# Kernel tuning notes

Hardware: AMD Instinct MI355X
Metric: run time of the kernel (lower is better)

The kernel has to match this reference:

```python
import jax, jax.numpy as jnp
import numpy as np

N = 50000      # nodes
E = 800000     # edges
D = 128        # in = out features (required by Euler residual update)
GRID_SIZE = 5
K = 3          # spline order
GRID_LO, GRID_HI = -1.0, 1.0
EPSILON = 0.001
NUM_BASES = GRID_SIZE + K  # 8


def make_grid(in_features):
    # extended uniform grid: [in, grid_size + 2k + 1]
    h = (GRID_HI - GRID_LO) / GRID_SIZE
    g = jnp.arange(-K, GRID_SIZE + K + 1, dtype=jnp.float32) * h + GRID_LO
    return jnp.broadcast_to(g, (in_features, g.shape[0]))


def b_splines(x, grid):
    # x: [N, in]; grid: [in, g+2k+1] -> bases: [N, in, g+k] (Cox-de Boor)
    xe = x[..., None]
    bases = ((xe >= grid[:, :-1]) & (xe < grid[:, 1:])).astype(x.dtype)
    for j in range(1, K + 1):
        left = (xe - grid[:, : -(j + 1)]) / (grid[:, j:-1] - grid[:, : -(j + 1)])
        right = (grid[:, j + 1:] - xe) / (grid[:, j + 1:] - grid[:, 1:-j])
        bases = left * bases[..., :-1] + right * bases[..., 1:]
    return bases


def kan_transform(x, base_w, spline_w, grid):
    # efficient-KAN layer (scale_and_bias=False): silu base branch + spline branch
    base = jax.nn.silu(x) @ base_w.T                    # [N, out]
    sb = b_splines(x, grid)                             # [N, in, g+k]
    spl = jnp.einsum('nib,oib->no', sb, spline_w)       # [N, out]
    return base + spl


def gcn_norm_coeffs(edge_index, n):
    # A_hat symmetric normalization: deg includes self-loop (+1)
    src, dst = edge_index[0], edge_index[1]
    deg = jnp.zeros((n,), jnp.float32).at[dst].add(1.0) + 1.0
    dis = jax.lax.rsqrt(deg)
    return dis[src] * dis[dst]


def setup_inputs() -> dict:
    key = jax.random.key(0)
    ks = jax.random.split(key, 6)
    x = jax.random.uniform(ks[0], (N, D), jnp.float32) * 2.0 - 1.0  # in grid_range
    edge_index = jax.random.randint(ks[1], (2, E), 0, N, dtype=jnp.int64)
    base_w_l = jax.random.normal(ks[2], (D, D), jnp.float32) * (1.0 / np.sqrt(D))
    spline_w_l = jax.random.normal(ks[3], (D, D, NUM_BASES), jnp.float32) * 0.1
    base_w_c = jax.random.normal(ks[4], (D, D), jnp.float32) * (1.0 / np.sqrt(D))
    spline_w_c = jax.random.normal(ks[5], (D, D, NUM_BASES), jnp.float32) * 0.1
    return {"x": x, "edge_index": edge_index, "base_w_l": base_w_l,
            "spline_w_l": spline_w_l, "base_w_c": base_w_c,
            "spline_w_c": spline_w_c, "delta_t": 2}


def reference(x, edge_index, base_w_l, spline_w_l, base_w_c, spline_w_c, delta_t):
    grid = make_grid(D)
    src, dst = edge_index[0], edge_index[1]
    norm = gcn_norm_coeffs(edge_index, N)  # [E]

    def layer(h):
        # KANLayer branch on node features
        h_l = kan_transform(h, base_w_l, spline_w_l, grid)
        # KANConv branch: aggregate_first -> normalized scatter-add, then KAN
        msgs = norm[:, None] * h[src]                              # [E, D]
        agg = jax.ops.segment_sum(msgs, dst, num_segments=N)       # [N, D]
        h_c = kan_transform(agg, base_w_c, spline_w_c, grid)
        return h_l + h_c

    for _ in range(int(delta_t)):   # explicit Euler ODE steps
        x = x + EPSILON * layer(x)
    return x
```

## Files before the change

kernel.cpp:

```cpp
#include <hip/hip_runtime.h>
#include <hip/hip_bf16.h>

#define NNODES 50000
#define NEDGES 800000
#define DF 128
#define KW 1152
#define EPS 0.001f
#define NB 196

typedef __bf16 bf16x8 __attribute__((ext_vector_type(8)));
typedef __bf16 bf16x4 __attribute__((ext_vector_type(4)));
typedef float  f32x4  __attribute__((ext_vector_type(4)));
typedef unsigned long ulongx2 __attribute__((ext_vector_type(2)));

#define GLOAD16(g, l) __builtin_amdgcn_global_load_lds( \
    (const __attribute__((address_space(1))) unsigned int*)(g), \
    (__attribute__((address_space(3))) unsigned int*)(l), 16, 0, 0)

__global__ void prep_fused(const float* __restrict__ x, const int* __restrict__ ei,
                           const float* __restrict__ bwl, const float* __restrict__ swl,
                           const float* __restrict__ bwc, const float* __restrict__ swc,
                           __bf16* __restrict__ xb, int* __restrict__ deg,
                           __bf16* __restrict__ wtl, __bf16* __restrict__ wtc) {
    const int bid = blockIdx.x;
    if (bid < 3125) {
        int i = bid * 256 + threadIdx.x;
        f32x4 a = ((const f32x4*)x)[2 * i];
        f32x4 b = ((const f32x4*)x)[2 * i + 1];
        bf16x8 o;
        o[0] = (__bf16)a[0]; o[1] = (__bf16)a[1]; o[2] = (__bf16)a[2]; o[3] = (__bf16)a[3];
        o[4] = (__bf16)b[0]; o[5] = (__bf16)b[1]; o[6] = (__bf16)b[2]; o[7] = (__bf16)b[3];
        ((bf16x8*)xb)[i] = o;
        atomicAdd(&deg[ei[NEDGES + i]], 1);
    } else {
        int idx = (bid - 3125) * 256 + threadIdx.x;
        int half = idx / (DF * KW);
        int gid  = idx - half * (DF * KW);
        const float* bw = half ? bwc : bwl;
        const float* sw = half ? swc : swl;
        __bf16*      wt = half ? wtc : wtl;
        int o = gid / KW;
        int k = gid - o * KW;
        float v = (k < 128) ? bw[o * DF + k] : sw[o * 1024 + (k - 128)];
        wt[gid] = (__bf16)v;
    }
}

__global__ void scan_part(const int* __restrict__ deg, int* __restrict__ bsum) {
    __shared__ int red[256];
    int t = threadIdx.x;
    int i = blockIdx.x * 256 + t;
    red[t] = (i < NNODES) ? deg[i] : 0;
    __syncthreads();
    for (int off = 128; off > 0; off >>= 1) {
        if (t < off) red[t] += red[t + off];
        __syncthreads();
    }
    if (t == 0) bsum[blockIdx.x] = red[0];
}

__global__ void scan_bsum(const int* __restrict__ bsum, int* __restrict__ boff) {
    __shared__ int buf[256];
    int t = threadIdx.x;
    int v = (t < NB) ? bsum[t] : 0;
    buf[t] = v;
    __syncthreads();
    for (int off = 1; off < 256; off <<= 1) {
        int x = (t >= off) ? buf[t - off] : 0;
        __syncthreads();
        buf[t] += x;
        __syncthreads();
    }
    if (t <= NB) boff[t] = buf[t] - ((t < NB) ? bsum[t] : 0);
}

__global__ void scan_final(const int* __restrict__ deg, const int* __restrict__ boff,
                           int* __restrict__ rowptr) {
    __shared__ int buf[256];
    int t = threadIdx.x;
    int i = blockIdx.x * 256 + t;
    int v = (i < NNODES) ? deg[i] : 0;
    buf[t] = v;
    __syncthreads();
    for (int off = 1; off < 256; off <<= 1) {
        int x = (t >= off) ? buf[t - off] : 0;
        __syncthreads();
        buf[t] += x;
        __syncthreads();
    }
    if (i < NNODES) rowptr[i] = buf[t] - v + boff[blockIdx.x];
    if (blockIdx.x == 0 && t == 0) rowptr[NNODES] = boff[NB];
}

__global__ void fill_csr(const int* __restrict__ ei, const int* __restrict__ deg,
                         const int* __restrict__ rowptr, int* __restrict__ cnt,
                         int* __restrict__ esrc, float* __restrict__ ew) {
    int e = blockIdx.x * 256 + threadIdx.x;
    if (e >= NEDGES) return;
    int s = ei[e];
    int d = ei[NEDGES + e];
    float w = rsqrtf((float)(deg[s] + 1)) * rsqrtf((float)(deg[d] + 1));
    int p = rowptr[d] + atomicAdd(&cnt[d], 1);
    esrc[p] = s;
    ew[p] = w;
}

__global__ __launch_bounds__(256) void agg_gather(
        const int* __restrict__ rowptr, const int* __restrict__ esrc,
        const float* __restrict__ ew, const __bf16* __restrict__ hb,
        __bf16* __restrict__ aggb) {
    const int tid = blockIdx.x * 256 + threadIdx.x;
    const int n = tid >> 4;
    const int l = tid & 15;
    if (n >= NNODES) return;
    int p  = rowptr[n];
    const int pe = rowptr[n + 1];
    float acc[8] = {};
    int   cs0, cs1, cs2, cs3;
    float cw0, cw1, cw2, cw3;
    bool have = (p + 3 < pe);
    if (have) {
        cs0 = esrc[p]; cs1 = esrc[p + 1]; cs2 = esrc[p + 2]; cs3 = esrc[p + 3];
        cw0 = ew[p];   cw1 = ew[p + 1];   cw2 = ew[p + 2];   cw3 = ew[p + 3];
    }
    while (have) {
        int np = p + 4;
        bool nh = (np + 3 < pe);
        int   ns0 = 0, ns1 = 0, ns2 = 0, ns3 = 0;
        float nw0 = 0, nw1 = 0, nw2 = 0, nw3 = 0;
        if (nh) {
            ns0 = esrc[np]; ns1 = esrc[np + 1]; ns2 = esrc[np + 2]; ns3 = esrc[np + 3];
            nw0 = ew[np];   nw1 = ew[np + 1];   nw2 = ew[np + 2];   nw3 = ew[np + 3];
        }
        bf16x8 v0 = *(const bf16x8*)(hb + (size_t)cs0 * DF + l * 8);
        bf16x8 v1 = *(const bf16x8*)(hb + (size_t)cs1 * DF + l * 8);
        bf16x8 v2 = *(const bf16x8*)(hb + (size_t)cs2 * DF + l * 8);
        bf16x8 v3 = *(const bf16x8*)(hb + (size_t)cs3 * DF + l * 8);
#pragma unroll
        for (int j = 0; j < 8; ++j)
            acc[j] += cw0 * (float)v0[j] + cw1 * (float)v1[j]
                    + cw2 * (float)v2[j] + cw3 * (float)v3[j];
        p = np;
        cs0 = ns0; cs1 = ns1; cs2 = ns2; cs3 = ns3;
        cw0 = nw0; cw1 = nw1; cw2 = nw2; cw3 = nw3;
        have = nh;
    }
    for (; p < pe; ++p) {
        int   s0 = esrc[p];
        float w0 = ew[p];
        bf16x8 v0 = *(const bf16x8*)(hb + (size_t)s0 * DF + l * 8);
#pragma unroll
        for (int j = 0; j < 8; ++j) acc[j] += w0 * (float)v0[j];
    }
    bf16x8 o;
#pragma unroll
    for (int j = 0; j < 8; ++j) o[j] = (__bf16)acc[j];
    *(bf16x8*)(aggb + (size_t)n * DF + l * 8) = o;
}

__global__ __launch_bounds__(256, 4) void kan_step(
        const float* __restrict__ h,
        const __bf16* __restrict__ xb,
        const __bf16* __restrict__ aggb,
        const __bf16* __restrict__ wtl, const __bf16* __restrict__ wtc,
        float* __restrict__ out, __bf16* __restrict__ outb) {
    __shared__ __bf16 Bs[3][128 * 32];
    __shared__ __bf16 Xs[64 * 128];

    const int tid  = threadIdx.x;
    const int lane = tid & 63;
    const int w    = tid >> 6;
    const int q    = lane >> 4, l15 = lane & 15;
    const int n0   = blockIdx.x * 64;
    const int myrow = w * 16 + l15;
    const int msw   = myrow & 7;

    const int relrow = lane >> 2;
    const int slotx  = (lane & 3) ^ ((relrow >> 1) & 3);
    const int r0 = w * 16 + relrow;
    const size_t gb0 = (size_t)r0 * KW + (size_t)slotx * 8;
    const size_t gb1 = gb0 + (size_t)64 * KW;

    const int bslot = (q ^ ((l15 >> 1) & 3)) * 8;

    const int xrow = tid >> 2, xseg = tid & 3;
    const bool xok = (n0 + xrow) < NNODES;
    const size_t xgoff = (size_t)(n0 + xrow) * DF + xseg * 32;

    f32x4 acc[8] = {};

    auto xs_write = [&](uint4 v0, uint4 v1, uint4 v2, uint4 v3) {
        const int gl = xrow * 16 + xseg * 4;
        const int sw = xrow & 7;
        *(uint4*)&Xs[(size_t)((gl + 0) ^ sw) * 8] = v0;
        *(uint4*)&Xs[(size_t)((gl + 1) ^ sw) * 8] = v1;
        *(uint4*)&Xs[(size_t)((gl + 2) ^ sw) * 8] = v2;
        *(uint4*)&Xs[(size_t)((gl + 3) ^ sw) * 8] = v3;
    };

    auto stageB = [&](int t2, int sb) {
        const __bf16* wtp = (t2 >= 36) ? wtc : wtl;
        const int k0 = ((t2 >= 36) ? t2 - 36 : t2) * 32;
        GLOAD16(wtp + gb0 + k0, &Bs[sb][(w * 16) * 32]);
        GLOAD16(wtp + gb1 + k0, &Bs[sb][(64 + w * 16) * 32]);
    };

    auto spline_pack = [&](float x) -> bf16x8 {
        float f  = __builtin_fmaf(x, 2.5f, 5.5f);
        float fi = floorf(f);
        int  idx = (int)fi;
        float u  = f - fi;
        float u2 = u * u, u3 = u2 * u;
        float om = 1.0f - u;
        float Wa = u3 * (1.0f / 6.0f);
        float Wb = (((-3.0f * u + 3.0f) * u + 3.0f) * u + 1.0f) * (1.0f / 6.0f);
        float Wc = ((3.0f * u - 6.0f) * u2 + 4.0f) * (1.0f / 6.0f);
        float Wd = om * om * om * (1.0f / 6.0f);
        unsigned long p =
              (unsigned long)__builtin_bit_cast(unsigned short, (__bf16)Wd)
            | ((unsigned long)__builtin_bit_cast(unsigned short, (__bf16)Wc) << 16)
            | ((unsigned long)__builtin_bit_cast(unsigned short, (__bf16)Wb) << 32)
            | ((unsigned long)__builtin_bit_cast(unsigned short, (__bf16)Wa) << 48);
        int tt = idx - 3;
        unsigned long lo, hi;
        if (tt >= 0) {
            int s = (tt & 3) * 16;
            unsigned long sv = p << s;
            unsigned long cr = (p >> (63 - s)) >> 1;
            bool hh = tt >= 4;
            lo = hh ? 0ul : sv;
            hi = hh ? sv : cr;
            if (tt >= 8) { lo = 0; hi = 0; }
        } else {
            int s = (-tt) * 16;
            lo = (tt >= -3) ? (p >> (s & 63)) : 0ul;
            hi = 0;
        }
        ulongx2 r; r[0] = lo; r[1] = hi;
        return __builtin_bit_cast(bf16x8, r);
    };

    auto silu8 = [&](const __bf16* xs) -> bf16x8 {
        bf16x8 v = *(const bf16x8*)xs;
        bf16x8 o;
#pragma unroll
        for (int j = 0; j < 8; ++j) {
            float x = (float)v[j];
            o[j] = (__bf16)(x / (1.0f + __expf(-x)));
        }
        return o;
    };

    uint4 a0 = {}, a1 = {}, a2 = {}, a3 = {};
    uint4 c0 = {}, c1 = {}, c2 = {}, c3 = {};
    if (xok) {
        const uint4* ga = (const uint4*)(xb + xgoff);
        a0 = ga[0]; a1 = ga[1]; a2 = ga[2]; a3 = ga[3];
        const uint4* gc = (const uint4*)(aggb + xgoff);
        c0 = gc[0]; c1 = gc[1]; c2 = gc[2]; c3 = gc[3];
    }
    xs_write(a0, a1, a2, a3);
    stageB(0, 0);
    stageB(1, 1);
    asm volatile("s_waitcnt lgkmcnt(0)" ::: "memory");

    auto body = [&](int t, int cb, int sb, bool doStage, bool last) {
        if (last) asm volatile("s_waitcnt vmcnt(0)" ::: "memory");
        else      asm volatile("s_waitcnt vmcnt(2)" ::: "memory");
        __builtin_amdgcn_s_barrier();
        __builtin_amdgcn_sched_barrier(0);

        if (t == 36) {
            xs_write(c0, c1, c2, c3);
            asm volatile("s_waitcnt lgkmcnt(0)" ::: "memory");
            __builtin_amdgcn_s_barrier();
            __builtin_amdgcn_sched_barrier(0);
        }

        if (doStage) stageB(t + 2, sb);

        const int ck = (t >= 36) ? t - 36 : t;
        bf16x8 a;
        if (ck < 4) {
            const int g = (myrow * 16 + ck * 4 + q) ^ msw;
            a = silu8(&Xs[(size_t)g * 8]);
        } else {
            const int f = (ck - 4) * 4 + q;
            const int g = (myrow * 16 + (f >> 3)) ^ msw;
            unsigned short u0 =
                *(const unsigned short*)&Xs[(size_t)g * 8 + (f & 7)];
            a = spline_pack(__builtin_bit_cast(float, (unsigned)u0 << 16));
        }

        bf16x8 bF[8];
#pragma unroll
        for (int nj = 0; nj < 8; ++nj)
            bF[nj] = *(const bf16x8*)&Bs[cb][(nj * 16 + l15) * 32 + bslot];
#pragma unroll
        for (int nj = 0; nj < 8; ++nj)
            acc[nj] = __builtin_amdgcn_mfma_f32_16x16x32_bf16(a, bF[nj], acc[nj], 0, 0, 0);
    };

    int cb = 0, sb = 2;
#pragma unroll 3
    for (int t = 0; t < 69; ++t) {
        body(t, cb, sb, true, false);
        cb = (cb == 2) ? 0 : cb + 1;
        sb = (sb == 2) ? 0 : sb + 1;
    }
    body(69, 0, 2, true,  false);
    body(70, 1, 0, false, false);
    body(71, 2, 0, false, true);

    const bool wxb = (outb != nullptr);
#pragma unroll
    for (int nj = 0; nj < 8; ++nj) {
#pragma unroll
        for (int r = 0; r < 4; ++r) {
            int row = n0 + w * 16 + q * 4 + r;
            int col = nj * 16 + l15;
            if (row < NNODES) {
                size_t idx = (size_t)row * DF + col;
                float v = h[idx] + EPS * acc[nj][r];
                out[idx] = v;
                if (wxb) outb[idx] = (__bf16)v;
            }
        }
    }
}

extern "C" void kernel_launch(void* const* d_in, const int* in_sizes, int n_in,
                              void* d_out, int out_size, void* d_ws, size_t ws_size,
                              hipStream_t stream) {
    const float* x   = (const float*)d_in[0];
    const int*   ei  = (const int*)d_in[1];
    const float* bwl = (const float*)d_in[2];
    const float* swl = (const float*)d_in[3];
    const float* bwc = (const float*)d_in[4];
    const float* swc = (const float*)d_in[5];
    float* out = (float*)d_out;

    char* ws = (char*)d_ws;
    int*    deg    = (int*)  (ws + 0);
    int*    cnt    = (int*)  (ws + 200000);
    int*    rowptr = (int*)  (ws + 400000);
    int*    bsum   = (int*)  (ws + 600064);
    int*    boff   = (int*)  (ws + 600896);
    int*    esrc   = (int*)  (ws + 601728);
    float*  ew     = (float*)(ws + 3801728);
    __bf16* xb     = (__bf16*)(ws + 7001728);
    __bf16* aggb   = (__bf16*)(ws + 19801728);
    __bf16* wtl    = (__bf16*)(ws + 32601728);
    __bf16* wtc    = (__bf16*)(ws + 32896640);

    (void)hipMemsetAsync(deg, 0, 400000, stream);
    prep_fused<<<4277, 256, 0, stream>>>(x, ei, bwl, swl, bwc, swc, xb, deg, wtl, wtc);
    scan_part<<<NB, 256, 0, stream>>>(deg, bsum);
    scan_bsum<<<1, 256, 0, stream>>>(bsum, boff);
    scan_final<<<NB, 256, 0, stream>>>(deg, boff, rowptr);
    fill_csr<<<3125, 256, 0, stream>>>(ei, deg, rowptr, cnt, esrc, ew);

    const int gemm_grid = (NNODES + 63) / 64;
    agg_gather<<<3125, 256, 0, stream>>>(rowptr, esrc, ew, xb, aggb);
    kan_step<<<gemm_grid, 256, 0, stream>>>(x, xb, aggb, wtl, wtc, out, xb);
    agg_gather<<<3125, 256, 0, stream>>>(rowptr, esrc, ew, xb, aggb);
    kan_step<<<gemm_grid, 256, 0, stream>>>(out, xb, aggb, wtl, wtc, out, (__bf16*)nullptr);
}
```

Baseline: 370.3 us.

## Co-schedule KAN-layer GEMM with edge aggregation in one interleaved kernel

Splits the combined KAN step into two parts. The node-feature KAN-layer GEMM, which needs no aggregation, now runs inside the gather kernel: one block in five does GEMM tiles while the others aggregate, so compute-bound and memory-bound work share the GPU. The result is stored as a bf16 partial sum. The second kernel then runs only the conv-branch GEMM and adds that partial at writeback. The cost is an extra bf16 round trip through global memory, rounding of the partial to bf16, and LDS allocated even for aggregation blocks, which may limit their occupancy.

```diff
diff --git a/kernel.cpp b/kernel.cpp
--- a/kernel.cpp
+++ b/kernel.cpp
@@ -9,7 +9,6 @@
 #define NB 196
 
 typedef __bf16 bf16x8 __attribute__((ext_vector_type(8)));
-typedef __bf16 bf16x4 __attribute__((ext_vector_type(4)));
 typedef float  f32x4  __attribute__((ext_vector_type(4)));
 typedef unsigned long ulongx2 __attribute__((ext_vector_type(2)));
 
@@ -105,64 +104,214 @@
     ew[p] = w;
 }
 
-__global__ __launch_bounds__(256) void agg_gather(
+__device__ __forceinline__ bf16x8 spline_pack(float x) {
+    float f  = __builtin_fmaf(x, 2.5f, 5.5f);
+    float fi = floorf(f);
+    int  idx = (int)fi;
+    float u  = f - fi;
+    float u2 = u * u, u3 = u2 * u;
+    float om = 1.0f - u;
+    float Wa = u3 * (1.0f / 6.0f);
+    float Wb = (((-3.0f * u + 3.0f) * u + 3.0f) * u + 1.0f) * (1.0f / 6.0f);
+    float Wc = ((3.0f * u - 6.0f) * u2 + 4.0f) * (1.0f / 6.0f);
+    float Wd = om * om * om * (1.0f / 6.0f);
+    unsigned long p =
+          (unsigned long)__builtin_bit_cast(unsigned short, (__bf16)Wd)
+        | ((unsigned long)__builtin_bit_cast(unsigned short, (__bf16)Wc) << 16)
+        | ((unsigned long)__builtin_bit_cast(unsigned short, (__bf16)Wb) << 32)
+        | ((unsigned long)__builtin_bit_cast(unsigned short, (__bf16)Wa) << 48);
+    int tt = idx - 3;
+    unsigned long lo, hi;
+    if (tt >= 0) {
+        int s = (tt & 3) * 16;
+        unsigned long sv = p << s;
+        unsigned long cr = (p >> (63 - s)) >> 1;
+        bool hh = tt >= 4;
+        lo = hh ? 0ul : sv;
+        hi = hh ? sv : cr;
+        if (tt >= 8) { lo = 0; hi = 0; }
+    } else {
+        int s = (-tt) * 16;
+        lo = (tt >= -3) ? (p >> (s & 63)) : 0ul;
+        hi = 0;
+    }
+    ulongx2 r; r[0] = lo; r[1] = hi;
+    return __builtin_bit_cast(bf16x8, r);
+}
+
+__device__ __forceinline__ bf16x8 silu8p(const __bf16* xs) {
+    bf16x8 v = *(const bf16x8*)xs;
+    bf16x8 o;
+#pragma unroll
+    for (int j = 0; j < 8; ++j) {
+        float x = (float)v[j];
+        o[j] = (__bf16)(x / (1.0f + __expf(-x)));
+    }
+    return o;
+}
+
+__global__ __launch_bounds__(256, 4) void agg_kanl(
         const int* __restrict__ rowptr, const int* __restrict__ esrc,
-        const float* __restrict__ ew, const __bf16* __restrict__ hb,
-        __bf16* __restrict__ aggb) {
-    const int tid = blockIdx.x * 256 + threadIdx.x;
-    const int n = tid >> 4;
-    const int l = tid & 15;
-    if (n >= NNODES) return;
-    int p  = rowptr[n];
-    const int pe = rowptr[n + 1];
-    float acc[8] = {};
-    int   cs0, cs1, cs2, cs3;
-    float cw0, cw1, cw2, cw3;
-    bool have = (p + 3 < pe);
-    if (have) {
-        cs0 = esrc[p]; cs1 = esrc[p + 1]; cs2 = esrc[p + 2]; cs3 = esrc[p + 3];
-        cw0 = ew[p];   cw1 = ew[p + 1];   cw2 = ew[p + 2];   cw3 = ew[p + 3];
-    }
-    while (have) {
-        int np = p + 4;
-        bool nh = (np + 3 < pe);
-        int   ns0 = 0, ns1 = 0, ns2 = 0, ns3 = 0;
-        float nw0 = 0, nw1 = 0, nw2 = 0, nw3 = 0;
-        if (nh) {
-            ns0 = esrc[np]; ns1 = esrc[np + 1]; ns2 = esrc[np + 2]; ns3 = esrc[np + 3];
-            nw0 = ew[np];   nw1 = ew[np + 1];   nw2 = ew[np + 2];   nw3 = ew[np + 3];
-        }
-        bf16x8 v0 = *(const bf16x8*)(hb + (size_t)cs0 * DF + l * 8);
-        bf16x8 v1 = *(const bf16x8*)(hb + (size_t)cs1 * DF + l * 8);
-        bf16x8 v2 = *(const bf16x8*)(hb + (size_t)cs2 * DF + l * 8);
-        bf16x8 v3 = *(const bf16x8*)(hb + (size_t)cs3 * DF + l * 8);
-#pragma unroll
-        for (int j = 0; j < 8; ++j)
-            acc[j] += cw0 * (float)v0[j] + cw1 * (float)v1[j]
-                    + cw2 * (float)v2[j] + cw3 * (float)v3[j];
-        p = np;
-        cs0 = ns0; cs1 = ns1; cs2 = ns2; cs3 = ns3;
-        cw0 = nw0; cw1 = nw1; cw2 = nw2; cw3 = nw3;
-        have = nh;
-    }
-    for (; p < pe; ++p) {
-        int   s0 = esrc[p];
-        float w0 = ew[p];
-        bf16x8 v0 = *(const bf16x8*)(hb + (size_t)s0 * DF + l * 8);
-#pragma unroll
-        for (int j = 0; j < 8; ++j) acc[j] += w0 * (float)v0[j];
-    }
-    bf16x8 o;
-#pragma unroll
-    for (int j = 0; j < 8; ++j) o[j] = (__bf16)acc[j];
-    *(bf16x8*)(aggb + (size_t)n * DF + l * 8) = o;
-}
-
-__global__ __launch_bounds__(256, 4) void kan_step(
+        const float* __restrict__ ew, const __bf16* __restrict__ xb,
+        __bf16* __restrict__ aggb, const __bf16* __restrict__ wtl,
+        __bf16* __restrict__ accb) {
+    __shared__ __bf16 Bs[3][128 * 32];
+    __shared__ __bf16 Xs[64 * 128];
+
+    const int bid = blockIdx.x;
+    const int k5 = bid / 5, r5 = bid - k5 * 5;
+    const bool isKanl = (r5 == 4) || (bid == 3906);
+
+    if (!isKanl) {
+        const int ablk = k5 * 4 + r5;
+        const int vtid = ablk * 256 + threadIdx.x;
+        const int n = vtid >> 4;
+        const int l = vtid & 15;
+        if (n >= NNODES) return;
+        int p  = rowptr[n];
+        const int pe = rowptr[n + 1];
+        float acc[8] = {};
+        int   cs0, cs1, cs2, cs3;
+        float cw0, cw1, cw2, cw3;
+        bool have = (p + 3 < pe);
+        if (have) {
+            cs0 = esrc[p]; cs1 = esrc[p + 1]; cs2 = esrc[p + 2]; cs3 = esrc[p + 3];
+            cw0 = ew[p];   cw1 = ew[p + 1];   cw2 = ew[p + 2];   cw3 = ew[p + 3];
+        }
+        while (have) {
+            int np = p + 4;
+            bool nh = (np + 3 < pe);
+            int   ns0 = 0, ns1 = 0, ns2 = 0, ns3 = 0;
+            float nw0 = 0, nw1 = 0, nw2 = 0, nw3 = 0;
+            if (nh) {
+                ns0 = esrc[np]; ns1 = esrc[np + 1]; ns2 = esrc[np + 2]; ns3 = esrc[np + 3];
+                nw0 = ew[np];   nw1 = ew[np + 1];   nw2 = ew[np + 2];   nw3 = ew[np + 3];
+            }
+            bf16x8 v0 = *(const bf16x8*)(xb + (size_t)cs0 * DF + l * 8);
+            bf16x8 v1 = *(const bf16x8*)(xb + (size_t)cs1 * DF + l * 8);
+            bf16x8 v2 = *(const bf16x8*)(xb + (size_t)cs2 * DF + l * 8);
+            bf16x8 v3 = *(const bf16x8*)(xb + (size_t)cs3 * DF + l * 8);
+#pragma unroll
+            for (int j = 0; j < 8; ++j)
+                acc[j] += cw0 * (float)v0[j] + cw1 * (float)v1[j]
+                        + cw2 * (float)v2[j] + cw3 * (float)v3[j];
+            p = np;
+            cs0 = ns0; cs1 = ns1; cs2 = ns2; cs3 = ns3;
+            cw0 = nw0; cw1 = nw1; cw2 = nw2; cw3 = nw3;
+            have = nh;
+        }
+        for (; p < pe; ++p) {
+            int   s0 = esrc[p];
+            float w0 = ew[p];
+            bf16x8 v0 = *(const bf16x8*)(xb + (size_t)s0 * DF + l * 8);
+#pragma unroll
+            for (int j = 0; j < 8; ++j) acc[j] += w0 * (float)v0[j];
+        }
+        bf16x8 o;
+#pragma unroll
+        for (int j = 0; j < 8; ++j) o[j] = (__bf16)acc[j];
+        *(bf16x8*)(aggb + (size_t)n * DF + l * 8) = o;
+        return;
+    }
+
+    const int kblk = (bid == 3906) ? 781 : k5;
+    const int tid  = threadIdx.x;
+    const int lane = tid & 63;
+    const int w    = tid >> 6;
+    const int q    = lane >> 4, l15 = lane & 15;
+    const int n0   = kblk * 64;
+    const int myrow = w * 16 + l15;
+    const int msw   = myrow & 7;
+
+    const int relrow = lane >> 2;
+    const int slotx  = (lane & 3) ^ ((relrow >> 1) & 3);
+    const int r0 = w * 16 + relrow;
+    const size_t gb0 = (size_t)r0 * KW + (size_t)slotx * 8;
+    const size_t gb1 = gb0 + (size_t)64 * KW;
+    const int bslot = (q ^ ((l15 >> 1) & 3)) * 8;
+
+    const int xrow = tid >> 2, xseg = tid & 3;
+    const bool xok = (n0 + xrow) < NNODES;
+    const size_t xgoff = (size_t)(n0 + xrow) * DF + xseg * 32;
+
+    f32x4 acc[8] = {};
+
+    auto stageB = [&](int t2, int sb) {
+        const int k0 = t2 * 32;
+        GLOAD16(wtl + gb0 + k0, &Bs[sb][(w * 16) * 32]);
+        GLOAD16(wtl + gb1 + k0, &Bs[sb][(64 + w * 16) * 32]);
+    };
+
+    {
+        uint4 a0 = {}, a1 = {}, a2 = {}, a3 = {};
+        if (xok) {
+            const uint4* ga = (const uint4*)(xb + xgoff);
+            a0 = ga[0]; a1 = ga[1]; a2 = ga[2]; a3 = ga[3];
+        }
+        const int gl = xrow * 16 + xseg * 4;
+        const int sw = xrow & 7;
+        *(uint4*)&Xs[(size_t)((gl + 0) ^ sw) * 8] = a0;
+        *(uint4*)&Xs[(size_t)((gl + 1) ^ sw) * 8] = a1;
+        *(uint4*)&Xs[(size_t)((gl + 2) ^ sw) * 8] = a2;
+        *(uint4*)&Xs[(size_t)((gl + 3) ^ sw) * 8] = a3;
+    }
+    stageB(0, 0);
+    stageB(1, 1);
+    asm volatile("s_waitcnt lgkmcnt(0)" ::: "memory");
+
+    auto body = [&](int t, int cb, int sb, bool doStage, bool last) {
+        if (last) asm volatile("s_waitcnt vmcnt(0)" ::: "memory");
+        else      asm volatile("s_waitcnt vmcnt(2)" ::: "memory");
+        __builtin_amdgcn_s_barrier();
+        __builtin_amdgcn_sched_barrier(0);
+        if (doStage) stageB(t + 2, sb);
+        bf16x8 a;
+        if (t < 4) {
+            const int g = (myrow * 16 + t * 4 + q) ^ msw;
+            a = silu8p(&Xs[(size_t)g * 8]);
+        } else {
+            const int f = (t - 4) * 4 + q;
+            const int g = (myrow * 16 + (f >> 3)) ^ msw;
+            unsigned short u0 = *(const unsigned short*)&Xs[(size_t)g * 8 + (f & 7)];
+            a = spline_pack(__builtin_bit_cast(float, (unsigned)u0 << 16));
+        }
+        bf16x8 bF[8];
+#pragma unroll
+        for (int nj = 0; nj < 8; ++nj)
+            bF[nj] = *(const bf16x8*)&Bs[cb][(nj * 16 + l15) * 32 + bslot];
+#pragma unroll
+        for (int nj = 0; nj < 8; ++nj)
+            acc[nj] = __builtin_amdgcn_mfma_f32_16x16x32_bf16(a, bF[nj], acc[nj], 0, 0, 0);
+    };
+
+    int cb = 0, sb = 2;
+#pragma unroll 3
+    for (int t = 0; t < 33; ++t) {
+        body(t, cb, sb, true, false);
+        cb = (cb == 2) ? 0 : cb + 1;
+        sb = (sb == 2) ? 0 : sb + 1;
+    }
+    body(33, 0, 2, true,  false);
+    body(34, 1, 0, false, false);
+    body(35, 2, 0, false, true);
+
+#pragma unroll
+    for (int nj = 0; nj < 8; ++nj) {
+#pragma unroll
+        for (int r = 0; r < 4; ++r) {
+            int row = n0 + w * 16 + q * 4 + r;
+            int col = nj * 16 + l15;
+            if (row < NNODES)
+                accb[(size_t)row * DF + col] = (__bf16)acc[nj][r];
+        }
+    }
+}
+
+__global__ __launch_bounds__(256, 4) void kan_c(
         const float* __restrict__ h,
-        const __bf16* __restrict__ xb,
         const __bf16* __restrict__ aggb,
-        const __bf16* __restrict__ wtl, const __bf16* __restrict__ wtc,
+        const __bf16* __restrict__ wtc,
+        const __bf16* __restrict__ accb,
         float* __restrict__ out, __bf16* __restrict__ outb) {
     __shared__ __bf16 Bs[3][128 * 32];
     __shared__ __bf16 Xs[64 * 128];
@@ -180,7 +329,6 @@
     const int r0 = w * 16 + relrow;
     const size_t gb0 = (size_t)r0 * KW + (size_t)slotx * 8;
     const size_t gb1 = gb0 + (size_t)64 * KW;
-
     const int bslot = (q ^ ((l15 >> 1) & 3)) * 8;
 
     const int xrow = tid >> 2, xseg = tid & 3;
@@ -189,77 +337,25 @@
 
     f32x4 acc[8] = {};
 
-    auto xs_write = [&](uint4 v0, uint4 v1, uint4 v2, uint4 v3) {
+    auto stageB = [&](int t2, int sb) {
+        const int k0 = t2 * 32;
+        GLOAD16(wtc + gb0 + k0, &Bs[sb][(w * 16) * 32]);
+        GLOAD16(wtc + gb1 + k0, &Bs[sb][(64 + w * 16) * 32]);
+    };
+
+    {
+        uint4 a0 = {}, a1 = {}, a2 = {}, a3 = {};
+        if (xok) {
+            const uint4* ga = (const uint4*)(aggb + xgoff);
+            a0 = ga[0]; a1 = ga[1]; a2 = ga[2]; a3 = ga[3];
+        }
         const int gl = xrow * 16 + xseg * 4;
         const int sw = xrow & 7;
-        *(uint4*)&Xs[(size_t)((gl + 0) ^ sw) * 8] = v0;
-        *(uint4*)&Xs[(size_t)((gl + 1) ^ sw) * 8] = v1;
-        *(uint4*)&Xs[(size_t)((gl + 2) ^ sw) * 8] = v2;
-        *(uint4*)&Xs[(size_t)((gl + 3) ^ sw) * 8] = v3;
-    };
-
-    auto stageB = [&](int t2, int sb) {
-        const __bf16* wtp = (t2 >= 36) ? wtc : wtl;
-        const int k0 = ((t2 >= 36) ? t2 - 36 : t2) * 32;
-        GLOAD16(wtp + gb0 + k0, &Bs[sb][(w * 16) * 32]);
-        GLOAD16(wtp + gb1 + k0, &Bs[sb][(64 + w * 16) * 32]);
-    };
-
-    auto spline_pack = [&](float x) -> bf16x8 {
-        float f  = __builtin_fmaf(x, 2.5f, 5.5f);
-        float fi = floorf(f);
-        int  idx = (int)fi;
-        float u  = f - fi;
-        float u2 = u * u, u3 = u2 * u;
-        float om = 1.0f - u;
-        float Wa = u3 * (1.0f / 6.0f);
-        float Wb = (((-3.0f * u + 3.0f) * u + 3.0f) * u + 1.0f) * (1.0f / 6.0f);
-        float Wc = ((3.0f * u - 6.0f) * u2 + 4.0f) * (1.0f / 6.0f);
-        float Wd = om * om * om * (1.0f / 6.0f);
-        unsigned long p =
-              (unsigned long)__builtin_bit_cast(unsigned short, (__bf16)Wd)
-            | ((unsigned long)__builtin_bit_cast(unsigned short, (__bf16)Wc) << 16)
-            | ((unsigned long)__builtin_bit_cast(unsigned short, (__bf16)Wb) << 32)
-            | ((unsigned long)__builtin_bit_cast(unsigned short, (__bf16)Wa) << 48);
-        int tt = idx - 3;
-        unsigned long lo, hi;
-        if (tt >= 0) {
-            int s = (tt & 3) * 16;
-            unsigned long sv = p << s;
-            unsigned long cr = (p >> (63 - s)) >> 1;
-            bool hh = tt >= 4;
-            lo = hh ? 0ul : sv;
-            hi = hh ? sv : cr;
-            if (tt >= 8) { lo = 0; hi = 0; }
-        } else {
-            int s = (-tt) * 16;
-            lo = (tt >= -3) ? (p >> (s & 63)) : 0ul;
-            hi = 0;
-        }
-        ulongx2 r; r[0] = lo; r[1] = hi;
-        return __builtin_bit_cast(bf16x8, r);
-    };
-
-    auto silu8 = [&](const __bf16* xs) -> bf16x8 {
-        bf16x8 v = *(const bf16x8*)xs;
-        bf16x8 o;
-#pragma unroll
-        for (int j = 0; j < 8; ++j) {
-            float x = (float)v[j];
-            o[j] = (__bf16)(x / (1.0f + __expf(-x)));
-        }
-        return o;
-    };
-
-    uint4 a0 = {}, a1 = {}, a2 = {}, a3 = {};
-    uint4 c0 = {}, c1 = {}, c2 = {}, c3 = {};
-    if (xok) {
-        const uint4* ga = (const uint4*)(xb + xgoff);
-        a0 = ga[0]; a1 = ga[1]; a2 = ga[2]; a3 = ga[3];
-        const uint4* gc = (const uint4*)(aggb + xgoff);
-        c0 = gc[0]; c1 = gc[1]; c2 = gc[2]; c3 = gc[3];
-    }
-    xs_write(a0, a1, a2, a3);
+        *(uint4*)&Xs[(size_t)((gl + 0) ^ sw) * 8] = a0;
+        *(uint4*)&Xs[(size_t)((gl + 1) ^ sw) * 8] = a1;
+        *(uint4*)&Xs[(size_t)((gl + 2) ^ sw) * 8] = a2;
+        *(uint4*)&Xs[(size_t)((gl + 3) ^ sw) * 8] = a3;
+    }
     stageB(0, 0);
     stageB(1, 1);
     asm volatile("s_waitcnt lgkmcnt(0)" ::: "memory");
@@ -269,29 +365,17 @@
         else      asm volatile("s_waitcnt vmcnt(2)" ::: "memory");
         __builtin_amdgcn_s_barrier();
         __builtin_amdgcn_sched_barrier(0);
-
-        if (t == 36) {
-            xs_write(c0, c1, c2, c3);
-            asm volatile("s_waitcnt lgkmcnt(0)" ::: "memory");
-            __builtin_amdgcn_s_barrier();
-            __builtin_amdgcn_sched_barrier(0);
-        }
-
         if (doStage) stageB(t + 2, sb);
-
-        const int ck = (t >= 36) ? t - 36 : t;
         bf16x8 a;
-        if (ck < 4) {
-            const int g = (myrow * 16 + ck * 4 + q) ^ msw;
-            a = silu8(&Xs[(size_t)g * 8]);
+        if (t < 4) {
+            const int g = (myrow * 16 + t * 4 + q) ^ msw;
+            a = silu8p(&Xs[(size_t)g * 8]);
         } else {
-            const int f = (ck - 4) * 4 + q;
+            const int f = (t - 4) * 4 + q;
             const int g = (myrow * 16 + (f >> 3)) ^ msw;
-            unsigned short u0 =
-                *(const unsigned short*)&Xs[(size_t)g * 8 + (f & 7)];
+            unsigned short u0 = *(const unsigned short*)&Xs[(size_t)g * 8 + (f & 7)];
             a = spline_pack(__builtin_bit_cast(float, (unsigned)u0 << 16));
         }
-
         bf16x8 bF[8];
 #pragma unroll
         for (int nj = 0; nj < 8; ++nj)
@@ -303,14 +387,14 @@
 
     int cb = 0, sb = 2;
 #pragma unroll 3
-    for (int t = 0; t < 69; ++t) {
+    for (int t = 0; t < 33; ++t) {
         body(t, cb, sb, true, false);
         cb = (cb == 2) ? 0 : cb + 1;
         sb = (sb == 2) ? 0 : sb + 1;
     }
-    body(69, 0, 2, true,  false);
-    body(70, 1, 0, false, false);
-    body(71, 2, 0, false, true);
+    body(33, 0, 2, true,  false);
+    body(34, 1, 0, false, false);
+    body(35, 2, 0, false, true);
 
     const bool wxb = (outb != nullptr);
 #pragma unroll
@@ -321,7 +405,7 @@
             int col = nj * 16 + l15;
             if (row < NNODES) {
                 size_t idx = (size_t)row * DF + col;
-                float v = h[idx] + EPS * acc[nj][r];
+                float v = h[idx] + EPS * (acc[nj][r] + (float)accb[idx]);
                 out[idx] = v;
                 if (wxb) outb[idx] = (__bf16)v;
             }
@@ -352,6 +436,7 @@
     __bf16* aggb   = (__bf16*)(ws + 19801728);
     __bf16* wtl    = (__bf16*)(ws + 32601728);
     __bf16* wtc    = (__bf16*)(ws + 32896640);
+    __bf16* accb   = (__bf16*)(ws + 33191552);
 
     (void)hipMemsetAsync(deg, 0, 400000, stream);
     prep_fused<<<4277, 256, 0, stream>>>(x, ei, bwl, swl, bwc, swc, xb, deg, wtl, wtc);
@@ -360,9 +445,8 @@
     scan_final<<<NB, 256, 0, stream>>>(deg, boff, rowptr);
     fill_csr<<<3125, 256, 0, stream>>>(ei, deg, rowptr, cnt, esrc, ew);
 
-    const int gemm_grid = (NNODES + 63) / 64;
-    agg_gather<<<3125, 256, 0, stream>>>(rowptr, esrc, ew, xb, aggb);
-    kan_step<<<gemm_grid, 256, 0, stream>>>(x, xb, aggb, wtl, wtc, out, xb);
-    agg_gather<<<3125, 256, 0, stream>>>(rowptr, esrc, ew, xb, aggb);
-    kan_step<<<gemm_grid, 256, 0, stream>>>(out, xb, aggb, wtl, wtc, out, (__bf16*)nullptr);
-}
+    agg_kanl<<<3907, 256, 0, stream>>>(rowptr, esrc, ew, xb, aggb, wtl, accb);
+    kan_c<<<782, 256, 0, stream>>>(x, aggb, wtc, accb, out, xb);
+    agg_kanl<<<3907, 256, 0, stream>>>(rowptr, esrc, ew, xb, aggb, wtl, accb);
+    kan_c<<<782, 256, 0, stream>>>(out, aggb, wtc, accb, out, (__bf16*)nullptr);
+}
```

New measurement: 374.2 us. Within noise of the previous version (+1.0%).
